# Optimization experiments

Hardware: AMD Instinct MI355X
Metric: run time of the kernel (lower is better)

Reference implementation:

```python
import jax, jax.numpy as jnp
import numpy as np
import math

NUM_HEADS = 16
HEAD_DIM = 128
HIDDEN = 2048
ROPE_THETA = 10000.0


def rotate_half(x):
    half = x.shape[-1] // 2
    return jnp.concatenate((-x[..., half:], x[..., :half]), axis=-1)


def rope_cos_sin(seq_len, dtype):
    # rotary_dim == head_dim (even)
    inv_freq = 1.0 / (ROPE_THETA ** (jnp.arange(0, HEAD_DIM, 2, dtype=jnp.float32) / HEAD_DIM))
    pos = jnp.arange(seq_len, dtype=jnp.float32)
    freqs = pos[:, None] * inv_freq[None, :]          # [S, HEAD_DIM/2]
    emb = jnp.concatenate((freqs, freqs), axis=-1)    # [S, HEAD_DIM]
    return jnp.cos(emb).astype(dtype), jnp.sin(emb).astype(dtype)


def setup_inputs() -> dict:
    key = jax.random.key(0)
    ks = jax.random.split(key, 5)
    B, S = 2, 2048
    scale = 1.0 / math.sqrt(HIDDEN)
    return {
        "hidden_states": jax.random.normal(ks[0], (B, S, HIDDEN), dtype=jnp.float32),
        "Wq": jax.random.normal(ks[1], (NUM_HEADS * HEAD_DIM, HIDDEN), dtype=jnp.float32) * scale,
        "Wk": jax.random.normal(ks[2], (NUM_HEADS * HEAD_DIM, HIDDEN), dtype=jnp.float32) * scale,
        "Wv": jax.random.normal(ks[3], (NUM_HEADS * HEAD_DIM, HIDDEN), dtype=jnp.float32) * scale,
        "Wo": jax.random.normal(ks[4], (HIDDEN, NUM_HEADS * HEAD_DIM), dtype=jnp.float32) * scale,
        "attention_mask": jnp.ones((B, S), dtype=bool),
    }


def reference(hidden_states, Wq, Wk, Wv, Wo, attention_mask):
    B, S, _ = hidden_states.shape
    # projections (Linear with weight [out, in]): y = x @ W.T
    def proj(W):
        y = jnp.einsum('bsh,oh->bso', hidden_states, W)
        return y.reshape(B, S, NUM_HEADS, HEAD_DIM).transpose(0, 2, 1, 3)  # [B,H,S,D]
    q, k, v = proj(Wq), proj(Wk), proj(Wv)

    cos, sin = rope_cos_sin(S, q.dtype)               # [S, D]
    cos = cos[None, None]                             # [1,1,S,D]
    sin = sin[None, None]
    q = q * cos + rotate_half(q) * sin
    k = k * cos + rotate_half(k) * sin

    scores = jnp.einsum('bhqd,bhkd->bhqk', q, k) / math.sqrt(HEAD_DIM)
    neg = jnp.finfo(scores.dtype).min
    causal = jnp.tril(jnp.ones((S, S), dtype=bool))   # past_len = 0
    scores = jnp.where(causal[None, None], scores, neg)
    key_mask = attention_mask[:, None, None, :]       # [B,1,1,S] bool
    scores = jnp.where(key_mask, scores, neg)

    attn = jax.nn.softmax(scores.astype(jnp.float32), axis=-1).astype(q.dtype)
    out = jnp.einsum('bhqk,bhkd->bhqd', attn, v)
    out = out.transpose(0, 2, 1, 3).reshape(B, S, NUM_HEADS * HEAD_DIM)
    return jnp.einsum('bso,ho->bsh', out, Wo)
```

## Files before the change

### kernel.cpp

```cpp
#include <hip/hip_runtime.h>
#include <stdint.h>

typedef unsigned short ushort_t;
typedef __attribute__((ext_vector_type(8))) __bf16 bf16x8;
typedef __attribute__((ext_vector_type(4))) float f32x4;

#define HIDDEN 2048
#define NHEADS 16
#define HDIM 128
#define SEQ 2048
#define BATCH 2
#define MROWS (BATCH*SEQ)

#define AS1 __attribute__((address_space(1)))
#define AS3 __attribute__((address_space(3)))

__device__ __forceinline__ ushort_t f2bf(float f) {
  uint32_t u = __float_as_uint(f);
  u += 0x7FFFu + ((u >> 16) & 1u);
  return (ushort_t)(u >> 16);
}
__device__ __forceinline__ float bf2f(ushort_t h) {
  return __uint_as_float((uint32_t)h << 16);
}

__device__ __forceinline__ f32x4 mfma16(bf16x8 a, bf16x8 b, f32x4 c) {
  return __builtin_amdgcn_mfma_f32_16x16x32_bf16(a, b, c, 0, 0, 0);
}

__global__ void cvt_kernel(const float* __restrict__ in, ushort_t* __restrict__ out,
                           float2* __restrict__ rotab, int n4) {
  int i = blockIdx.x * blockDim.x + threadIdx.x;
  if (i < n4) {
    float4 v = ((const float4*)in)[i];
    uint32_t lo = (uint32_t)f2bf(v.x) | ((uint32_t)f2bf(v.y) << 16);
    uint32_t hi = (uint32_t)f2bf(v.z) | ((uint32_t)f2bf(v.w) << 16);
    ((uint2*)out)[i] = make_uint2(lo, hi);
  }
  if (i < SEQ * 64) {
    int s = i >> 6, dl = i & 63;
    float th = exp2f((float)dl * -0.2076205059304601f);
    float sn, cs;
    sincosf((float)s * th, &sn, &cs);
    rotab[i] = make_float2(cs, sn);
  }
}

__global__ void cvt4_kernel(const float* __restrict__ w0, const float* __restrict__ w1,
                            const float* __restrict__ w2, const float* __restrict__ w3,
                            ushort_t* __restrict__ o0, ushort_t* __restrict__ o1,
                            ushort_t* __restrict__ o2, ushort_t* __restrict__ o3) {
  int y = blockIdx.y;
  const float* in = (y == 0) ? w0 : (y == 1) ? w1 : (y == 2) ? w2 : w3;
  ushort_t* out = (y == 0) ? o0 : (y == 1) ? o1 : (y == 2) ? o2 : o3;
  int i = blockIdx.x * blockDim.x + threadIdx.x;
  float4 v = ((const float4*)in)[i];
  uint32_t lo = (uint32_t)f2bf(v.x) | ((uint32_t)f2bf(v.y) << 16);
  uint32_t hi = (uint32_t)f2bf(v.z) | ((uint32_t)f2bf(v.w) << 16);
  ((uint2*)out)[i] = make_uint2(lo, hi);
}

__device__ __forceinline__ void gemm128_core(const ushort_t* __restrict__ Ag,
                                             const ushort_t* __restrict__ Bg,
                                             ushort_t* As, ushort_t* Bs,
                                             f32x4 acc[4][4], int tid) {
  const int lane = tid & 63, wv = tid >> 6;
  const int r4 = lane >> 2;
  const int c8 = (((lane & 3) ^ ((r4 >> 1) & 3)) << 3);
  const int wm = (wv >> 1) * 64, wn = (wv & 1) * 64;
  const int mq = lane & 15, quad = lane >> 4;
  const int sw = (mq >> 1) & 3;

  auto stage = [&](int k0, int buf) {
#pragma unroll
    for (int cc = 0; cc < 2; ++cc) {
      int chunk = wv + cc * 4;
      const ushort_t* ga = Ag + (size_t)(chunk * 16 + r4) * HIDDEN + k0 + c8;
      const ushort_t* gb = Bg + (size_t)(chunk * 16 + r4) * HIDDEN + k0 + c8;
      __builtin_amdgcn_global_load_lds((AS1 void*)ga, (AS3 void*)(As + buf * 4096 + chunk * 512), 16, 0, 0);
      __builtin_amdgcn_global_load_lds((AS1 void*)gb, (AS3 void*)(Bs + buf * 4096 + chunk * 512), 16, 0, 0);
    }
  };

  stage(0, 0);
  __syncthreads();
#pragma unroll 1
  for (int k0 = 0; k0 < HIDDEN; k0 += 32) {
    const int cur = (k0 >> 5) & 1;
    if (k0 + 32 < HIDDEN) stage(k0 + 32, cur ^ 1);
    const ushort_t* A = As + cur * 4096;
    const ushort_t* B = Bs + cur * 4096;
    bf16x8 a[4], b[4];
#pragma unroll
    for (int i = 0; i < 4; ++i)
      a[i] = *(const bf16x8*)(A + (wm + i * 16 + mq) * 32 + ((quad ^ sw) << 3));
#pragma unroll
    for (int j = 0; j < 4; ++j)
      b[j] = *(const bf16x8*)(B + (wn + j * 16 + mq) * 32 + ((quad ^ sw) << 3));
#pragma unroll
    for (int i = 0; i < 4; ++i)
#pragma unroll
      for (int j = 0; j < 4; ++j)
        acc[i][j] = mfma16(a[i], b[j], acc[i][j]);
    __syncthreads();
  }
}


#define QKV_PHASE_MFMA(MH, NH, BB)                                                  \
  __builtin_amdgcn_s_barrier();                                                     \
  asm volatile("s_waitcnt lgkmcnt(0)" ::: "memory");                                \
  __builtin_amdgcn_s_setprio(1);                                                    \
  _Pragma("unroll") for (int f_ = 0; f_ < 4; ++f_)                                  \
  _Pragma("unroll") for (int n_ = 0; n_ < 2; ++n_)                                  \
  _Pragma("unroll") for (int kk_ = 0; kk_ < 2; ++kk_)                               \
    acc[(MH)*4+f_][(NH)*2+n_] =                                                     \
      mfma16(af[f_*2+kk_], BB[n_*2+kk_], acc[(MH)*4+f_][(NH)*2+n_]);                \
  __builtin_amdgcn_s_setprio(0);

#define QKV_TILE(CB, NB, KT)                                                        \
  {                                                                                 \
    const ushort_t* A_ = lds_q + (CB);                                              \
    const ushort_t* B_ = lds_q + (CB) + 16384;                                      \
    _Pragma("unroll") for (int u = 0; u < 8; ++u) af[u] = *(const bf16x8*)(A_ + aoff[u]); \
    _Pragma("unroll") for (int u = 0; u < 4; ++u) b0r[u] = *(const bf16x8*)(B_ + boff[u]); \
    stageA((KT), 0, (NB));                                                          \
    QKV_PHASE_MFMA(0, 0, b0r)                                                       \
    asm volatile("s_waitcnt vmcnt(4)" ::: "memory");                                \
    __builtin_amdgcn_s_barrier();                                                   \
    _Pragma("unroll") for (int u = 0; u < 4; ++u) b1r[u] = *(const bf16x8*)(B_ + 8192 + boff[u]); \
    stageB((KT), 0, (NB));                                                          \
    QKV_PHASE_MFMA(0, 1, b1r)                                                       \
    asm volatile("s_waitcnt vmcnt(4)" ::: "memory");                                \
    __builtin_amdgcn_s_barrier();                                                   \
    _Pragma("unroll") for (int u = 0; u < 8; ++u) af[u] = *(const bf16x8*)(A_ + 8192 + aoff[u]); \
    stageB((KT), 1, (NB));                                                          \
    QKV_PHASE_MFMA(1, 1, b1r)                                                       \
    __builtin_amdgcn_s_barrier();                                                   \
    stageA((KT), 1, (NB));                                                          \
    QKV_PHASE_MFMA(1, 0, b0r)                                                       \
    asm volatile("s_waitcnt vmcnt(4)" ::: "memory");                                \
    __builtin_amdgcn_s_barrier();                                                   \
  }

#define QKV_TAIL(CB)                                                                \
  {                                                                                 \
    const ushort_t* A_ = lds_q + (CB);                                              \
    const ushort_t* B_ = lds_q + (CB) + 16384;                                      \
    _Pragma("unroll") for (int u = 0; u < 8; ++u) af[u] = *(const bf16x8*)(A_ + aoff[u]); \
    _Pragma("unroll") for (int u = 0; u < 4; ++u) b0r[u] = *(const bf16x8*)(B_ + boff[u]); \
    QKV_PHASE_MFMA(0, 0, b0r)                                                       \
    asm volatile("s_waitcnt vmcnt(2)" ::: "memory");                                \
    __builtin_amdgcn_s_barrier();                                                   \
    _Pragma("unroll") for (int u = 0; u < 4; ++u) b1r[u] = *(const bf16x8*)(B_ + 8192 + boff[u]); \
    QKV_PHASE_MFMA(0, 1, b1r)                                                       \
    asm volatile("s_waitcnt vmcnt(0)" ::: "memory");                                \
    __builtin_amdgcn_s_barrier();                                                   \
    _Pragma("unroll") for (int u = 0; u < 8; ++u) af[u] = *(const bf16x8*)(A_ + 8192 + aoff[u]); \
    QKV_PHASE_MFMA(1, 1, b1r)                                                       \
    __builtin_amdgcn_s_barrier();                                                   \
    QKV_PHASE_MFMA(1, 0, b0r)                                                       \
  }

__global__ __launch_bounds__(512, 2) void qkv_gemm(const ushort_t* __restrict__ X,
                                                   const ushort_t* __restrict__ Wq,
                                                   const ushort_t* __restrict__ Wk,
                                                   const ushort_t* __restrict__ Wv,
                                                   const float2* __restrict__ RoTab,
                                                   ushort_t* __restrict__ Q,
                                                   ushort_t* __restrict__ K,
                                                   ushort_t* __restrict__ Vt) {
  __shared__ __align__(16) ushort_t lds_q[65536];

  const int tid = threadIdx.x, lane = tid & 63, wv = tid >> 6;
  const int wr = wv >> 2, wc = wv & 3;
  const int mq = lane & 15, quad = lane >> 4;
  const int lr = lane >> 3;
  const int csw = ((lane & 7) ^ (lr & 7)) * 8;

  const int lin = blockIdx.x;
  const int xcd = lin & 7, s = lin >> 3;
  const int by = xcd * 3 + (s % 3);
  const int bx = s / 3;
  const int m0 = bx * 256;
  const int nglob = by * 256;
  const int which = nglob >> 11;
  const int n0 = nglob & 2047;
  const ushort_t* Ag = X + (size_t)m0 * HIDDEN;
  const ushort_t* Bg = ((which == 0) ? Wq : (which == 1) ? Wk : Wv) + (size_t)n0 * HIDDEN;

  int aoff[8], boff[4];
#pragma unroll
  for (int f = 0; f < 4; ++f)
#pragma unroll
    for (int kk = 0; kk < 2; ++kk)
      aoff[f * 2 + kk] = (f * 32 + wr * 16 + mq) * 64 + (((kk * 4 + quad) ^ (mq & 7)) * 8);
#pragma unroll
  for (int n = 0; n < 2; ++n)
#pragma unroll
    for (int kk = 0; kk < 2; ++kk)
      boff[n * 2 + kk] = (n * 64 + wc * 16 + mq) * 64 + (((kk * 4 + quad) ^ (mq & 7)) * 8);

  auto stageA = [&](int kt, int half, int nb) {
#pragma unroll
    for (int i = 0; i < 2; ++i) {
      int seg = wv + i * 8;
      const ushort_t* src = Ag + (size_t)(half * 128 + seg * 8 + lr) * HIDDEN + kt * 64 + csw;
      __builtin_amdgcn_global_load_lds((AS1 void*)src,
                                       (AS3 void*)(lds_q + nb + half * 8192 + seg * 512), 16, 0, 0);
    }
  };
  auto stageB = [&](int kt, int half, int nb) {
#pragma unroll
    for (int i = 0; i < 2; ++i) {
      int seg = wv + i * 8;
      const ushort_t* src = Bg + (size_t)(half * 128 + seg * 8 + lr) * HIDDEN + kt * 64 + csw;
      __builtin_amdgcn_global_load_lds((AS1 void*)src,
                                       (AS3 void*)(lds_q + nb + 16384 + half * 8192 + seg * 512), 16, 0, 0);
    }
  };

  f32x4 acc[8][4];
  const f32x4 zf = {0.f, 0.f, 0.f, 0.f};
#pragma unroll
  for (int i = 0; i < 8; ++i)
#pragma unroll
    for (int j = 0; j < 4; ++j) acc[i][j] = zf;

  bf16x8 af[8], b0r[4], b1r[4];

  stageA(0, 0, 0);
  stageB(0, 0, 0);
  stageB(0, 1, 0);
  stageA(0, 1, 0);
  __syncthreads();

#pragma unroll 1
  for (int tp = 0; tp < 15; ++tp) {
    QKV_TILE(0, 32768, 2 * tp + 1)
    QKV_TILE(32768, 0, 2 * tp + 2)
  }
  QKV_TILE(0, 32768, 31)
  QKV_TAIL(32768)

  if (which != 2) {
    ushort_t* dst = (which == 0) ? Q : K;
    const float qscale = (which == 0) ? 0.08838834764831845f : 1.0f;
    const int dl = wc * 16 + mq;
#pragma unroll
    for (int a = 0; a < 8; ++a) {
#pragma unroll
      for (int r = 0; r < 4; ++r) {
        int mrow = m0 + (a >> 2) * 128 + (a & 3) * 32 + wr * 16 + quad * 4 + r;
        int bb = mrow >> 11, sq = mrow & (SEQ - 1);
        float2 t = RoTab[(sq << 6) + dl];
        float cs = t.x, sn = t.y;
#pragma unroll
        for (int cp = 0; cp < 2; ++cp) {
          float lo = acc[a][cp * 2][r], hi = acc[a][cp * 2 + 1][r];
          float nlo = (lo * cs - hi * sn) * qscale;
          float nhi = (hi * cs + lo * sn) * qscale;
          int ocol = n0 + cp * 128 + dl;
          int hh = ocol >> 7;
          size_t base = ((size_t)(bb * NHEADS + hh) * SEQ + sq) * HDIM + dl;
          dst[base]      = f2bf(nlo);
          dst[base + 64] = f2bf(nhi);
        }
      }
    }
  } else {
    __syncthreads();
#pragma unroll
    for (int a = 0; a < 8; ++a)
#pragma unroll
      for (int c4 = 0; c4 < 4; ++c4) {
        int cc = (c4 >> 1) * 128 + (c4 & 1) * 64 + wc * 16 + mq;
        int mb = (a >> 2) * 128 + (a & 3) * 32 + wr * 16 + quad * 4;
        uint32_t lo = (uint32_t)f2bf(acc[a][c4][0]) | ((uint32_t)f2bf(acc[a][c4][1]) << 16);
        uint32_t hi = (uint32_t)f2bf(acc[a][c4][2]) | ((uint32_t)f2bf(acc[a][c4][3]) << 16);
        *(uint2*)(lds_q + cc * 256 + (mb ^ ((cc & 7) * 8))) = make_uint2(lo, hi);
      }
    __syncthreads();
    const int bb = m0 >> 11, sq0 = m0 & (SEQ - 1);
#pragma unroll
    for (int it = 0; it < 16; ++it) {
      int cc = it * 16 + (tid >> 5);
      int sc = tid & 31;
      uint4 v = *(const uint4*)(lds_q + cc * 256 + ((sc ^ (cc & 7)) * 8));
      int hh = (n0 + cc) >> 7, d = (n0 + cc) & (HDIM - 1);
      *(uint4*)(Vt + ((size_t)(bb * NHEADS + hh) * HDIM + d) * SEQ + sq0 + sc * 8) = v;
    }
  }
}

__global__ __launch_bounds__(256, 1) void flash_kernel(const ushort_t* __restrict__ Q,
                                                       const ushort_t* __restrict__ K,
                                                       const ushort_t* __restrict__ Vt,
                                                       ushort_t* __restrict__ Ao) {
  __shared__ __align__(16) ushort_t sK[2][64 * 128];
  __shared__ __align__(16) ushort_t sV[2][128 * 64];
  __shared__ __align__(16) ushort_t sP[128 * 64];
  ushort_t* sO = &sK[0][0];

  const int tid = threadIdx.x, lane = tid & 63, wv = tid >> 6;
  const int lq = lane & 15, quad = lane >> 4;
  const int lin = blockIdx.x;
  const int xcd = lin & 7, slot = lin >> 3;
  const int bh = xcd * 4 + (slot & 3);
  const int pair = slot >> 2;
  const ushort_t* Qb = Q + (size_t)bh * SEQ * HDIM;
  const ushort_t* Kb = K + (size_t)bh * SEQ * HDIM;
  const ushort_t* Vb = Vt + (size_t)bh * HDIM * SEQ;
  const int b = bh >> 4, h = bh & 15;

  auto stageK = [&](int j, ushort_t* dst) {
    int rr = lane >> 4, g = lane & 15;
#pragma unroll
    for (int t = 0; t < 4; ++t) {
      int chunk = wv * 4 + t;
      int row = chunk * 4 + rr;
      int gs = (g ^ (row & 7)) * 8;
      __builtin_amdgcn_global_load_lds((AS1 void*)(Kb + (size_t)(j * 64 + row) * HDIM + gs),
                                       (AS3 void*)(dst + chunk * 512), 16, 0, 0);
    }
  };
  auto stageV = [&](int j, ushort_t* dst) {
    int rr = lane >> 3, g = lane & 7;
#pragma unroll
    for (int t = 0; t < 4; ++t) {
      int chunk = wv * 4 + t;
      int row = chunk * 8 + rr;
      int gs = (g ^ (row & 7)) * 8;
      __builtin_amdgcn_global_load_lds((AS1 void*)(Vb + (size_t)row * SEQ + j * 64 + gs),
                                       (AS3 void*)(dst + chunk * 512), 16, 0, 0);
    }
  };

  const f32x4 zf = {0.f, 0.f, 0.f, 0.f};

#pragma unroll 1
  for (int phase = 0; phase < 2; ++phase) {
    const int T = phase ? (15 - pair) : pair;
    const int nsteps = 2 * T + 2;

    bf16x8 qf[2][4];
#pragma unroll
    for (int n = 0; n < 2; ++n)
#pragma unroll
      for (int kt = 0; kt < 4; ++kt)
        qf[n][kt] = *(const bf16x8*)(Qb + (size_t)(T * 128 + wv * 32 + n * 16 + lq) * HDIM +
                                     kt * 32 + quad * 8);

    float m_i[2] = {-1e30f, -1e30f}, l_i[2] = {0.f, 0.f};
    f32x4 oacc[8][2];
#pragma unroll
    for (int m = 0; m < 8; ++m)
#pragma unroll
      for (int n = 0; n < 2; ++n) oacc[m][n] = zf;

    __syncthreads();
    stageK(0, sK[0]);
    stageV(0, sV[0]);
    __syncthreads();

#pragma unroll 1
    for (int j = 0; j < nsteps; ++j) {
      const int cur = j & 1;
      if (j + 1 < nsteps) {
        stageK(j + 1, sK[cur ^ 1]);
        stageV(j + 1, sV[cur ^ 1]);
      }

      const ushort_t* sKc = sK[cur];
      f32x4 sacc[4][2];
#pragma unroll
      for (int m = 0; m < 4; ++m)
#pragma unroll
        for (int n = 0; n < 2; ++n) sacc[m][n] = zf;
#pragma unroll
      for (int kt = 0; kt < 4; ++kt) {
        bf16x8 kf[4];
#pragma unroll
        for (int m = 0; m < 4; ++m) {
          int row = m * 16 + lq;
          kf[m] = *(const bf16x8*)(sKc + row * 128 + (((kt * 4 + quad) ^ (row & 7)) * 8));
        }
#pragma unroll
        for (int m = 0; m < 4; ++m)
#pragma unroll
          for (int n = 0; n < 2; ++n)
            sacc[m][n] = mfma16(kf[m], qf[n][kt], sacc[m][n]);
      }

      const bool diag = (j >= 2 * T);
#pragma unroll
      for (int n = 0; n < 2; ++n) {
        const int qr = wv * 32 + n * 16 + lq;
        if (diag) {
          const int rowg = T * 128 + qr;
#pragma unroll
          for (int m = 0; m < 4; ++m)
#pragma unroll
            for (int r = 0; r < 4; ++r) {
              int key = j * 64 + m * 16 + quad * 4 + r;
              if (key > rowg) sacc[m][n][r] = -1e30f;
            }
        }
        float rm = -1e30f;
#pragma unroll
        for (int m = 0; m < 4; ++m)
#pragma unroll
          for (int r = 0; r < 4; ++r) rm = fmaxf(rm, sacc[m][n][r]);
        rm = fmaxf(rm, __shfl_xor(rm, 16, 64));
        rm = fmaxf(rm, __shfl_xor(rm, 32, 64));
        float mnew = fmaxf(m_i[n], rm);
        float alpha = __expf(m_i[n] - mnew);
        m_i[n] = mnew;
        float rs = 0.f;
#pragma unroll
        for (int m = 0; m < 4; ++m)
#pragma unroll
          for (int r = 0; r < 4; ++r) {
            float p = __expf(sacc[m][n][r] - mnew);
            sacc[m][n][r] = p;
            rs += p;
          }
        rs += __shfl_xor(rs, 16, 64);
        rs += __shfl_xor(rs, 32, 64);
        l_i[n] = l_i[n] * alpha + rs;
#pragma unroll
        for (int m = 0; m < 8; ++m)
#pragma unroll
          for (int r = 0; r < 4; ++r) oacc[m][n][r] *= alpha;
#pragma unroll
        for (int m = 0; m < 4; ++m) {
          uint32_t lo = (uint32_t)f2bf(sacc[m][n][0]) | ((uint32_t)f2bf(sacc[m][n][1]) << 16);
          uint32_t hi = (uint32_t)f2bf(sacc[m][n][2]) | ((uint32_t)f2bf(sacc[m][n][3]) << 16);
          int gw = m * 2 + (quad >> 1);
          *(uint2*)(sP + qr * 64 + ((gw ^ (qr & 7)) * 8) + (quad & 1) * 4) = make_uint2(lo, hi);
        }
      }

      const ushort_t* sVc = sV[cur];
#pragma unroll
      for (int kt = 0; kt < 2; ++kt) {
        bf16x8 pf[2];
#pragma unroll
        for (int n = 0; n < 2; ++n) {
          int qr = wv * 32 + n * 16 + lq;
          pf[n] = *(const bf16x8*)(sP + qr * 64 + (((kt * 4 + quad) ^ (qr & 7)) * 8));
        }
#pragma unroll
        for (int m = 0; m < 8; ++m) {
          int d = m * 16 + lq;
          bf16x8 vf = *(const bf16x8*)(sVc + d * 64 + (((kt * 4 + quad) ^ (d & 7)) * 8));
#pragma unroll
          for (int n = 0; n < 2; ++n)
            oacc[m][n] = mfma16(vf, pf[n], oacc[m][n]);
        }
      }

      __syncthreads();
    }

    float inv0 = 1.f / l_i[0], inv1 = 1.f / l_i[1];
#pragma unroll
    for (int n = 0; n < 2; ++n) {
      float inv = n ? inv1 : inv0;
      int qr = wv * 32 + n * 16 + lq;
#pragma unroll
      for (int m = 0; m < 8; ++m) {
        uint32_t lo = (uint32_t)f2bf(oacc[m][n][0] * inv) | ((uint32_t)f2bf(oacc[m][n][1] * inv) << 16);
        uint32_t hi = (uint32_t)f2bf(oacc[m][n][2] * inv) | ((uint32_t)f2bf(oacc[m][n][3] * inv) << 16);
        int gw = m * 2 + (quad >> 1);
        *(uint2*)(sO + qr * 128 + ((gw ^ (qr & 7)) * 8) + (quad & 1) * 4) = make_uint2(lo, hi);
      }
    }
    __syncthreads();
#pragma unroll
    for (int it = 0; it < 8; ++it) {
      int qr = it * 16 + (tid >> 4);
      int g = tid & 15;
      uint4 v = *(const uint4*)(sO + qr * 128 + ((g ^ (qr & 7)) * 8));
      *(uint4*)(Ao + ((size_t)(b * SEQ + T * 128 + qr)) * (NHEADS * HDIM) + h * HDIM + g * 8) = v;
    }
  }
}

__global__ __launch_bounds__(256) void out_gemm(const ushort_t* __restrict__ Ain,
                                                const ushort_t* __restrict__ Wo,
                                                float* __restrict__ Y) {
  __shared__ __align__(16) ushort_t As[2][128 * 32];
  __shared__ __align__(16) ushort_t Bs[2][128 * 32];
  const int tid = threadIdx.x;
  const int lin = blockIdx.x;
  const int xcd = lin & 7, s = lin >> 3;
  const int by = xcd + 8 * (s & 1);
  const int bx = s >> 1;
  const int m0 = bx * 128;
  const int n0 = by * 128;

  f32x4 acc[4][4];
  const f32x4 zf = {0.f, 0.f, 0.f, 0.f};
#pragma unroll
  for (int i = 0; i < 4; ++i)
#pragma unroll
    for (int j = 0; j < 4; ++j) acc[i][j] = zf;

  gemm128_core(Ain + (size_t)m0 * HIDDEN, Wo + (size_t)n0 * HIDDEN, &As[0][0], &Bs[0][0], acc, tid);

  const int lane = tid & 63, wv = tid >> 6;
  const int wm = (wv >> 1) * 64, wn = (wv & 1) * 64;
  const int mq = lane & 15, quad = lane >> 4;
#pragma unroll
  for (int i = 0; i < 4; ++i)
#pragma unroll
    for (int j = 0; j < 4; ++j)
#pragma unroll
      for (int r = 0; r < 4; ++r) {
        int m = m0 + wm + i * 16 + quad * 4 + r;
        int o = n0 + wn + j * 16 + mq;
        Y[(size_t)m * HIDDEN + o] = acc[i][j][r];
      }
}

extern "C" void kernel_launch(void* const* d_in, const int* in_sizes, int n_in,
                              void* d_out, int out_size, void* d_ws, size_t ws_size,
                              hipStream_t stream) {
  const float* hs = (const float*)d_in[0];
  const float* Wq = (const float*)d_in[1];
  const float* Wk = (const float*)d_in[2];
  const float* Wv = (const float*)d_in[3];
  const float* Wo = (const float*)d_in[4];
  float* out = (float*)d_out;

  ushort_t* ws  = (ushort_t*)d_ws;
  ushort_t* Xb  = ws;
  ushort_t* Wqb = Xb  + (size_t)MROWS * HIDDEN;
  ushort_t* Wkb = Wqb + (size_t)HIDDEN * HIDDEN;
  ushort_t* Wvb = Wkb + (size_t)HIDDEN * HIDDEN;
  ushort_t* Wob = Wvb + (size_t)HIDDEN * HIDDEN;
  ushort_t* Qb  = Wob + (size_t)HIDDEN * HIDDEN;
  ushort_t* Kb  = Qb  + (size_t)MROWS * HIDDEN;
  ushort_t* Vtb = Kb  + (size_t)MROWS * HIDDEN;
  ushort_t* Ao  = Vtb + (size_t)MROWS * HIDDEN;
  float2*   RoTab = (float2*)(Ao + (size_t)MROWS * HIDDEN);

  cvt_kernel<<<(MROWS * HIDDEN / 4) / 256, 256, 0, stream>>>(hs, Xb, RoTab, MROWS * HIDDEN / 4);
  cvt4_kernel<<<dim3((HIDDEN * HIDDEN / 4) / 256, 4), 256, 0, stream>>>(
      Wq, Wk, Wv, Wo, Wqb, Wkb, Wvb, Wob);

  qkv_gemm<<<dim3(384), 512, 0, stream>>>(Xb, Wqb, Wkb, Wvb, RoTab, Qb, Kb, Vtb);
  flash_kernel<<<dim3(256), 256, 0, stream>>>(Qb, Kb, Vtb, Ao);
  out_gemm<<<dim3(512), 256, 0, stream>>>(Ao, Wob, out);
}
```

Measured before the change: 395.8 us.

## Run both causal query tiles concurrently in one 512-thread flash block sharing K/V stages

The flash kernel previously processed its two query tiles (pair and 15-pair) sequentially with 256 threads. Now 8 waves split into two groups, each handling one tile at the same time, sharing double-buffered K/V LDS loads, with per-group P and output staging. The short tile's group idles through the extra steps but still joins barriers. This doubles waves per CU and reuses K/V tiles across both query tiles, at the cost of more LDS and idle waves in the short group.

```diff
diff --git a/kernel.cpp b/kernel.cpp
--- a/kernel.cpp
+++ b/kernel.cpp
@@ -293,21 +293,27 @@
   }
 }
 
-__global__ __launch_bounds__(256, 1) void flash_kernel(const ushort_t* __restrict__ Q,
+__global__ __launch_bounds__(512, 1) void flash_kernel(const ushort_t* __restrict__ Q,
                                                        const ushort_t* __restrict__ K,
                                                        const ushort_t* __restrict__ Vt,
                                                        ushort_t* __restrict__ Ao) {
-  __shared__ __align__(16) ushort_t sK[2][64 * 128];
-  __shared__ __align__(16) ushort_t sV[2][128 * 64];
-  __shared__ __align__(16) ushort_t sP[128 * 64];
-  ushort_t* sO = &sK[0][0];
-
+  __shared__ __align__(16) ushort_t smem[49152];
   const int tid = threadIdx.x, lane = tid & 63, wv = tid >> 6;
+  const int grp = wv >> 2, wg = wv & 3;
   const int lq = lane & 15, quad = lane >> 4;
   const int lin = blockIdx.x;
   const int xcd = lin & 7, slot = lin >> 3;
   const int bh = xcd * 4 + (slot & 3);
-  const int pair = slot >> 2;
+  const int p = slot >> 2;
+  const int T = grp ? (15 - p) : p;
+  const int nsteps = 2 * T + 2;
+  const int jmax = 32 - 2 * p;
+  ushort_t* sKb0 = smem;
+  ushort_t* sKb1 = smem + 8192;
+  ushort_t* sVb0 = smem + 16384;
+  ushort_t* sVb1 = smem + 24576;
+  ushort_t* sP   = smem + 32768 + grp * 8192;
+
   const ushort_t* Qb = Q + (size_t)bh * SEQ * HDIM;
   const ushort_t* Kb = K + (size_t)bh * SEQ * HDIM;
   const ushort_t* Vb = Vt + (size_t)bh * HDIM * SEQ;
@@ -316,8 +322,8 @@
   auto stageK = [&](int j, ushort_t* dst) {
     int rr = lane >> 4, g = lane & 15;
 #pragma unroll
-    for (int t = 0; t < 4; ++t) {
-      int chunk = wv * 4 + t;
+    for (int t = 0; t < 2; ++t) {
+      int chunk = wv * 2 + t;
       int row = chunk * 4 + rr;
       int gs = (g ^ (row & 7)) * 8;
       __builtin_amdgcn_global_load_lds((AS1 void*)(Kb + (size_t)(j * 64 + row) * HDIM + gs),
@@ -327,8 +333,8 @@
   auto stageV = [&](int j, ushort_t* dst) {
     int rr = lane >> 3, g = lane & 7;
 #pragma unroll
-    for (int t = 0; t < 4; ++t) {
-      int chunk = wv * 4 + t;
+    for (int t = 0; t < 2; ++t) {
+      int chunk = wv * 2 + t;
       int row = chunk * 8 + rr;
       int gs = (g ^ (row & 7)) * 8;
       __builtin_amdgcn_global_load_lds((AS1 void*)(Vb + (size_t)row * SEQ + j * 64 + gs),
@@ -338,40 +344,36 @@
 
   const f32x4 zf = {0.f, 0.f, 0.f, 0.f};
 
+  bf16x8 qf[2][4];
+#pragma unroll
+  for (int n = 0; n < 2; ++n)
+#pragma unroll
+    for (int kt = 0; kt < 4; ++kt)
+      qf[n][kt] = *(const bf16x8*)(Qb + (size_t)(T * 128 + wg * 32 + n * 16 + lq) * HDIM +
+                                   kt * 32 + quad * 8);
+
+  float m_i[2] = {-1e30f, -1e30f}, l_i[2] = {0.f, 0.f};
+  f32x4 oacc[8][2];
+#pragma unroll
+  for (int m = 0; m < 8; ++m)
+#pragma unroll
+    for (int n = 0; n < 2; ++n) oacc[m][n] = zf;
+
+  stageK(0, sKb0);
+  stageV(0, sVb0);
+  __syncthreads();
+
 #pragma unroll 1
-  for (int phase = 0; phase < 2; ++phase) {
-    const int T = phase ? (15 - pair) : pair;
-    const int nsteps = 2 * T + 2;
-
-    bf16x8 qf[2][4];
-#pragma unroll
-    for (int n = 0; n < 2; ++n)
-#pragma unroll
-      for (int kt = 0; kt < 4; ++kt)
-        qf[n][kt] = *(const bf16x8*)(Qb + (size_t)(T * 128 + wv * 32 + n * 16 + lq) * HDIM +
-                                     kt * 32 + quad * 8);
-
-    float m_i[2] = {-1e30f, -1e30f}, l_i[2] = {0.f, 0.f};
-    f32x4 oacc[8][2];
-#pragma unroll
-    for (int m = 0; m < 8; ++m)
-#pragma unroll
-      for (int n = 0; n < 2; ++n) oacc[m][n] = zf;
-
-    __syncthreads();
-    stageK(0, sK[0]);
-    stageV(0, sV[0]);
-    __syncthreads();
-
-#pragma unroll 1
-    for (int j = 0; j < nsteps; ++j) {
-      const int cur = j & 1;
-      if (j + 1 < nsteps) {
-        stageK(j + 1, sK[cur ^ 1]);
-        stageV(j + 1, sV[cur ^ 1]);
-      }
-
-      const ushort_t* sKc = sK[cur];
+  for (int j = 0; j < jmax; ++j) {
+    const int cur = j & 1;
+    const ushort_t* sKc = cur ? sKb1 : sKb0;
+    const ushort_t* sVc = cur ? sVb1 : sVb0;
+    if (j + 1 < jmax) {
+      stageK(j + 1, cur ? sKb0 : sKb1);
+      stageV(j + 1, cur ? sVb0 : sVb1);
+    }
+
+    if (j < nsteps) {
       f32x4 sacc[4][2];
 #pragma unroll
       for (int m = 0; m < 4; ++m)
@@ -395,7 +397,7 @@
       const bool diag = (j >= 2 * T);
 #pragma unroll
       for (int n = 0; n < 2; ++n) {
-        const int qr = wv * 32 + n * 16 + lq;
+        const int qr = wg * 32 + n * 16 + lq;
         if (diag) {
           const int rowg = T * 128 + qr;
 #pragma unroll
@@ -421,9 +423,9 @@
         for (int m = 0; m < 4; ++m)
 #pragma unroll
           for (int r = 0; r < 4; ++r) {
-            float p = __expf(sacc[m][n][r] - mnew);
-            sacc[m][n][r] = p;
-            rs += p;
+            float pz = __expf(sacc[m][n][r] - mnew);
+            sacc[m][n][r] = pz;
+            rs += pz;
           }
         rs += __shfl_xor(rs, 16, 64);
         rs += __shfl_xor(rs, 32, 64);
@@ -441,13 +443,12 @@
         }
       }
 
-      const ushort_t* sVc = sV[cur];
 #pragma unroll
       for (int kt = 0; kt < 2; ++kt) {
         bf16x8 pf[2];
 #pragma unroll
         for (int n = 0; n < 2; ++n) {
-          int qr = wv * 32 + n * 16 + lq;
+          int qr = wg * 32 + n * 16 + lq;
           pf[n] = *(const bf16x8*)(sP + qr * 64 + (((kt * 4 + quad) ^ (qr & 7)) * 8));
         }
 #pragma unroll
@@ -459,28 +460,32 @@
             oacc[m][n] = mfma16(vf, pf[n], oacc[m][n]);
         }
       }
-
-      __syncthreads();
-    }
-
-    float inv0 = 1.f / l_i[0], inv1 = 1.f / l_i[1];
-#pragma unroll
-    for (int n = 0; n < 2; ++n) {
-      float inv = n ? inv1 : inv0;
-      int qr = wv * 32 + n * 16 + lq;
-#pragma unroll
-      for (int m = 0; m < 8; ++m) {
-        uint32_t lo = (uint32_t)f2bf(oacc[m][n][0] * inv) | ((uint32_t)f2bf(oacc[m][n][1] * inv) << 16);
-        uint32_t hi = (uint32_t)f2bf(oacc[m][n][2] * inv) | ((uint32_t)f2bf(oacc[m][n][3] * inv) << 16);
-        int gw = m * 2 + (quad >> 1);
-        *(uint2*)(sO + qr * 128 + ((gw ^ (qr & 7)) * 8) + (quad & 1) * 4) = make_uint2(lo, hi);
-      }
-    }
+    }
+
     __syncthreads();
+  }
+
+  ushort_t* sO = smem + grp * 16384;
+  float inv0 = 1.f / l_i[0], inv1 = 1.f / l_i[1];
+#pragma unroll
+  for (int n = 0; n < 2; ++n) {
+    float inv = n ? inv1 : inv0;
+    int qr = wg * 32 + n * 16 + lq;
+#pragma unroll
+    for (int m = 0; m < 8; ++m) {
+      uint32_t lo = (uint32_t)f2bf(oacc[m][n][0] * inv) | ((uint32_t)f2bf(oacc[m][n][1] * inv) << 16);
+      uint32_t hi = (uint32_t)f2bf(oacc[m][n][2] * inv) | ((uint32_t)f2bf(oacc[m][n][3] * inv) << 16);
+      int gw = m * 2 + (quad >> 1);
+      *(uint2*)(sO + qr * 128 + ((gw ^ (qr & 7)) * 8) + (quad & 1) * 4) = make_uint2(lo, hi);
+    }
+  }
+  __syncthreads();
+  {
+    const int ltid = tid & 255;
 #pragma unroll
     for (int it = 0; it < 8; ++it) {
-      int qr = it * 16 + (tid >> 4);
-      int g = tid & 15;
+      int qr = it * 16 + (ltid >> 4);
+      int g = ltid & 15;
       uint4 v = *(const uint4*)(sO + qr * 128 + ((g ^ (qr & 7)) * 8));
       *(uint4*)(Ao + ((size_t)(b * SEQ + T * 128 + qr)) * (NHEADS * HDIM) + h * HDIM + g * 8) = v;
     }
@@ -551,6 +556,6 @@
       Wq, Wk, Wv, Wo, Wqb, Wkb, Wvb, Wob);
 
   qkv_gemm<<<dim3(384), 512, 0, stream>>>(Xb, Wqb, Wkb, Wvb, RoTab, Qb, Kb, Vtb);
-  flash_kernel<<<dim3(256), 256, 0, stream>>>(Qb, Kb, Vtb, Ao);
+  flash_kernel<<<dim3(256), 512, 0, stream>>>(Qb, Kb, Vtb, Ao);
   out_gemm<<<dim3(512), 256, 0, stream>>>(Ao, Wob, out);
 }
```

Result: faster. 374.7 us (-5.3%).
